# Performance work log

Hardware: AMD Instinct MI355X
Metric: run time of the kernel (lower is better)

## Reference

```python
import jax, jax.numpy as jnp
import numpy as np

B, T, D, H = 8, 1024, 768, 12
HD = D // H          # 64 head dim
WINDOW = 768         # sliding-window width hardcoded in the block
EPS = 1e-5

def _layer_norm(x, w, b):
    mu = jnp.mean(x, axis=-1, keepdims=True)
    var = jnp.mean(jnp.square(x - mu), axis=-1, keepdims=True)
    return (x - mu) * jax.lax.rsqrt(var + EPS) * w + b

def setup_inputs() -> dict:
    key = jax.random.key(0)
    ks = jax.random.split(key, 16)
    s = 0.02
    return {
        "x": jax.random.normal(ks[0], (B, T, D), jnp.float32),
        "attn_mask": jnp.ones((B, T), jnp.int32),
        "ln1_w": jnp.ones((D,), jnp.float32),
        "ln1_b": jnp.zeros((D,), jnp.float32),
        "w_attn": jax.random.normal(ks[1], (D, 3 * D), jnp.float32) * s,
        "b_attn": jnp.zeros((3 * D,), jnp.float32),
        "w_proj": jax.random.normal(ks[2], (D, D), jnp.float32) * s,
        "b_proj": jnp.zeros((D,), jnp.float32),
        "ln2_w": jnp.ones((D,), jnp.float32),
        "ln2_b": jnp.zeros((D,), jnp.float32),
        "w_fc": jax.random.normal(ks[3], (D, 4 * D), jnp.float32) * s,
        "b_fc": jnp.zeros((4 * D,), jnp.float32),
        "w_fc_proj": jax.random.normal(ks[4], (4 * D, D), jnp.float32) * s,
        "b_fc_proj": jnp.zeros((D,), jnp.float32),
    }

def reference(x, attn_mask, ln1_w, ln1_b, w_attn, b_attn, w_proj, b_proj,
              ln2_w, ln2_b, w_fc, b_fc, w_fc_proj, b_fc_proj):
    dtype = x.dtype
    # --- attention sub-block ---
    x1 = _layer_norm(x, ln1_w, ln1_b)
    qkv = x1 @ w_attn + b_attn                       # [B,T,3D]
    q, k, v = jnp.split(qkv, 3, axis=-1)
    q = q.reshape(B, T, H, HD).transpose(0, 2, 1, 3)  # [B,H,T,HD]
    k = k.reshape(B, T, H, HD).transpose(0, 2, 1, 3)
    v = v.reshape(B, T, H, HD).transpose(0, 2, 1, 3)
    # causal + sliding-window + padding mask (additive bias, as in source)
    i = jnp.arange(T)[:, None]
    j = jnp.arange(T)[None, :]
    keep = (j <= i) & (j >= i - WINDOW + 1)           # [T,T]
    keep = keep[None, None] & (attn_mask.astype(bool))[:, None, None, :]  # [B,1,T,T]
    mask_bias = jnp.where(keep, jnp.zeros((), dtype), jnp.full((), jnp.finfo(dtype).min, dtype))
    scale = 1.0 / np.sqrt(HD)
    scores = jnp.einsum('bhqd,bhkd->bhqk', q, k) * scale + mask_bias
    probs = jax.nn.softmax(scores, axis=-1)
    attn = jnp.einsum('bhqk,bhkd->bhqd', probs, v)    # [B,H,T,HD]
    attn = attn.transpose(0, 2, 1, 3).reshape(B, T, D)
    a = attn @ w_proj + b_proj
    x = x + a
    # --- MLP sub-block ---
    x3 = _layer_norm(x, ln2_w, ln2_b)
    h = jax.nn.gelu(x3 @ w_fc + b_fc, approximate=False)
    m = h @ w_fc_proj + b_fc_proj
    return x + m
```

## Files before the change

kernel.cpp:

```cpp
#include <hip/hip_runtime.h>
#include <hip/hip_bf16.h>
#include <math.h>

#define NB 8
#define NT 1024
#define ND 768
#define NH 12
#define HD 64
#define WINDOW 768
#define LN_EPS 1e-5f
#define NEGF -3.4028234663852886e38f
#define SCL2 0.18033688011112042f

static const int BT = NB * NT;

typedef __bf16 bf16x8 __attribute__((ext_vector_type(8)));
typedef float  f32x4  __attribute__((ext_vector_type(4)));
typedef unsigned short ushort_t;

__device__ __forceinline__ unsigned short f2bf(float f) {
    __hip_bfloat16 h = __float2bfloat16(f);
    return __builtin_bit_cast(unsigned short, h);
}

__device__ __forceinline__ void load_lds16(const void* g, void* l) {
    __builtin_amdgcn_global_load_lds((const __attribute__((address_space(1))) unsigned int*)g,
                                     (__attribute__((address_space(3))) unsigned int*)l,
                                     16, 0, 0);
}

__global__ __launch_bounds__(256) void transpose_all(const float* __restrict__ w0, ushort_t* __restrict__ t0v,
                                                     const float* __restrict__ w1, ushort_t* __restrict__ t1v,
                                                     const float* __restrict__ w2, ushort_t* __restrict__ t2v,
                                                     const float* __restrict__ w3, ushort_t* __restrict__ t3v) {
    int bid = blockIdx.x;
    const float* w; ushort_t* wt; int K, N;
    if (bid < 1728)                    { w = w0; wt = t0v; K = 768;  N = 2304; }
    else if ((bid -= 1728) < 576)      { w = w1; wt = t1v; K = 768;  N = 768;  }
    else if ((bid -= 576) < 2304)      { w = w2; wt = t2v; K = 768;  N = 3072; }
    else       { bid -= 2304;            w = w3; wt = t3v; K = 3072; N = 768;  }
    const int nxt = N / 32;
    const int n0 = (bid % nxt) * 32, k0 = (bid / nxt) * 32;
    __shared__ float t[32][33];
    const int tx = threadIdx.x & 31, ty = threadIdx.x >> 5;
    for (int r = ty; r < 32; r += 8)
        t[r][tx] = w[(size_t)(k0 + r) * N + n0 + tx];
    __syncthreads();
    for (int r = ty; r < 32; r += 8)
        wt[(size_t)(n0 + r) * K + k0 + tx] = f2bf(t[tx][r]);
}

__global__ __launch_bounds__(256) void transpose_v(const ushort_t* __restrict__ qkvb,
                                                   ushort_t* __restrict__ vT) {
    const int t0 = blockIdx.x * 64;
    const int h = blockIdx.y, b = blockIdx.z;
    __shared__ ushort_t sm[64 * 72];
    const int tid = threadIdx.x;
    #pragma unroll
    for (int p = 0; p < 2; p++) {
        int idx = p * 256 + tid;
        int r = idx >> 3, c = idx & 7;
        *(bf16x8*)&sm[r * 72 + c * 8] =
            *(const bf16x8*)(qkvb + (size_t)(b * NT + t0 + r) * (3 * ND) + 2 * ND + h * HD + c * 8);
    }
    __syncthreads();
    #pragma unroll
    for (int p = 0; p < 2; p++) {
        int idx = p * 256 + tid;
        int d = idx >> 3, c2 = idx & 7;
        ushort_t tmp[8];
        #pragma unroll
        for (int j = 0; j < 8; j++) {
            int kp = c2 * 8 + j;
            int key = ((kp & 1) << 4) | ((kp >> 1) & 15) | (kp & 32);
            tmp[j] = sm[key * 72 + d];
        }
        *(bf16x8*)(vT + ((size_t)((b * NH + h) * HD + d)) * NT + t0 + c2 * 8) = *(bf16x8*)tmp;
    }
}

__global__ __launch_bounds__(256) void ln_kernel(const float* __restrict__ x,
                                                 const float* __restrict__ w,
                                                 const float* __restrict__ b,
                                                 ushort_t* __restrict__ out) {
    const int row  = blockIdx.x * 4 + (threadIdx.x >> 6);
    const int lane = threadIdx.x & 63;
    const float* xr = x + (size_t)row * ND;

    float4 v[3];
    #pragma unroll
    for (int s = 0; s < 3; s++) v[s] = *(const float4*)(xr + s * 256 + lane * 4);

    float sum = 0.f;
    #pragma unroll
    for (int s = 0; s < 3; s++) sum += v[s].x + v[s].y + v[s].z + v[s].w;
    #pragma unroll
    for (int off = 1; off < 64; off <<= 1) sum += __shfl_xor(sum, off, 64);
    const float mu = sum * (1.0f / ND);

    float var = 0.f;
    #pragma unroll
    for (int s = 0; s < 3; s++) {
        float a0 = v[s].x - mu, a1 = v[s].y - mu, a2 = v[s].z - mu, a3 = v[s].w - mu;
        var += a0 * a0 + a1 * a1 + a2 * a2 + a3 * a3;
    }
    #pragma unroll
    for (int off = 1; off < 64; off <<= 1) var += __shfl_xor(var, off, 64);
    const float rstd = rsqrtf(var * (1.0f / ND) + LN_EPS);

    #pragma unroll
    for (int s = 0; s < 3; s++) {
        const int col = s * 256 + lane * 4;
        float4 w4 = *(const float4*)(w + col);
        float4 b4 = *(const float4*)(b + col);
        ushort4 r;
        r.x = f2bf((v[s].x - mu) * rstd * w4.x + b4.x);
        r.y = f2bf((v[s].y - mu) * rstd * w4.y + b4.y);
        r.z = f2bf((v[s].z - mu) * rstd * w4.z + b4.z);
        r.w = f2bf((v[s].w - mu) * rstd * w4.w + b4.w);
        *(ushort4*)(out + (size_t)row * ND + col) = r;
    }
}

template <int EPI>
__global__ __launch_bounds__(256) void gemm_bt(const ushort_t* __restrict__ A,
                                               const ushort_t* __restrict__ Bt,
                                               const float* __restrict__ bias,
                                               const float* __restrict__ resid,
                                               void* __restrict__ Cout,
                                               int M, int N, int K) {
    __shared__ __align__(16) ushort_t smem[2][2][128 * 32];

    const int tid  = threadIdx.x;
    const int bm   = blockIdx.y * 128;
    const int bn   = blockIdx.x * 128;
    const int lane = tid & 63;
    const int wave = tid >> 6;
    const int wm   = (wave & 1) * 64;
    const int wn   = (wave >> 1) * 64;
    const int fcol = lane & 15;
    const int quad = lane >> 4;

    f32x4 acc[4][4] = {};

    const int srow = tid >> 2, scg = (tid & 3) * 8;

    auto issue = [&](int k0, int buf) {
        #pragma unroll
        for (int p = 0; p < 2; p++) {
            const int row = srow + p * 64;
            const int flat = (p * 256 + tid) * 8;
            load_lds16(A  + (size_t)(bm + row) * K + k0 + scg, &smem[buf][0][flat]);
            load_lds16(Bt + (size_t)(bn + row) * K + k0 + scg, &smem[buf][1][flat]);
        }
    };

    issue(0, 0);
    const int KT = K >> 5;
    for (int kt = 0; kt < KT; kt++) {
        const int cur = kt & 1;
        __syncthreads();
        if (kt + 1 < KT) issue((kt + 1) << 5, cur ^ 1);

        bf16x8 a[4], b[4];
        #pragma unroll
        for (int i = 0; i < 4; i++)
            a[i] = *(const bf16x8*)&smem[cur][0][(wm + i * 16 + fcol) * 32 + quad * 8];
        #pragma unroll
        for (int j = 0; j < 4; j++)
            b[j] = *(const bf16x8*)&smem[cur][1][(wn + j * 16 + fcol) * 32 + quad * 8];
        #pragma unroll
        for (int i = 0; i < 4; i++)
            #pragma unroll
            for (int j = 0; j < 4; j++)
                acc[i][j] = __builtin_amdgcn_mfma_f32_16x16x32_bf16(a[i], b[j], acc[i][j], 0, 0, 0);
    }

    if (EPI == 1) {
        #pragma unroll
        for (int j = 0; j < 4; j++) {
            const int gcol = bn + wn + j * 16 + fcol;
            const float bs = bias[gcol];
            #pragma unroll
            for (int i = 0; i < 4; i++) {
                #pragma unroll
                for (int r = 0; r < 4; r++) {
                    const int grow = bm + wm + i * 16 + quad * 4 + r;
                    float val = acc[i][j][r] + bs + resid[(size_t)grow * N + gcol];
                    ((float*)Cout)[(size_t)grow * N + gcol] = val;
                }
            }
        }
    } else {
        __syncthreads();
        ushort_t* Cs = &smem[0][0][0] + wave * (64 * 40);
        #pragma unroll
        for (int hh = 0; hh < 2; hh++) {
            #pragma unroll
            for (int jj = 0; jj < 2; jj++) {
                const int j = hh * 2 + jj;
                const float bs = bias[bn + wn + j * 16 + fcol];
                #pragma unroll
                for (int i = 0; i < 4; i++) {
                    #pragma unroll
                    for (int r = 0; r < 4; r++) {
                        float val = acc[i][j][r] + bs;
                        if (EPI == 2) {
                            float y = 0.7978845608028654f * (val + 0.044715f * val * val * val);
                            float t = 1.0f - 2.0f / (1.0f + __expf(2.0f * y));
                            val = 0.5f * val * (1.0f + t);
                        }
                        const int lr = i * 16 + quad * 4 + r;
                        Cs[lr * 40 + jj * 16 + fcol] = f2bf(val);
                    }
                }
            }
            #pragma unroll
            for (int p = 0; p < 4; p++) {
                const int cid = p * 64 + lane;
                const int lr = cid >> 2, ck = cid & 3;
                bf16x8 vv = *(const bf16x8*)&Cs[lr * 40 + ck * 8];
                *(bf16x8*)((ushort_t*)Cout + (size_t)(bm + wm + lr) * N + bn + wn + hh * 32 + ck * 8) = vv;
            }
        }
    }
}

__global__ __launch_bounds__(256) void flash_attn_mfma(const ushort_t* __restrict__ qkvb,
                                                       const ushort_t* __restrict__ vT,
                                                       const int* __restrict__ amask,
                                                       ushort_t* __restrict__ out) {
    const int qt = 15 - blockIdx.x;
    const int h  = blockIdx.y;
    const int b  = blockIdx.z;
    const int q0 = qt * 64;

    __shared__ __align__(16) ushort_t QPs[64 * 64];
    __shared__ __align__(16) ushort_t Ks[2][64 * 64];
    __shared__ __align__(16) ushort_t Vts[2][64 * 64];

    const int tid  = threadIdx.x;
    const int lane = tid & 63;
    const int wave = tid >> 6;
    const int fcol = lane & 15;
    const int quad = lane >> 4;
    const int wq0  = wave * 16;

    #pragma unroll
    for (int p = 0; p < 2; p++) {
        int flat = p * 256 + tid;
        int r = flat >> 3, c = (flat & 7) ^ (r & 7);
        load_lds16(qkvb + (size_t)(b * NT + q0 + r) * (3 * ND) + h * HD + c * 8, &QPs[flat * 8]);
    }
    __syncthreads();

    bf16x8 aQ[2];
    {
        const int qr = wq0 + fcol;
        #pragma unroll
        for (int ks = 0; ks < 2; ks++) {
            int c = ks * 4 + quad;
            aQ[ks] = *(const bf16x8*)&QPs[qr * 64 + ((c ^ (qr & 7)) * 8)];
        }
    }

    bf16x8 bones;
    #pragma unroll
    for (int i = 0; i < 8; i++) bones[i] = (__bf16)1.0f;

    auto issueKV = [&](int cch, int buf) {
        const int kbase = cch * 64;
        #pragma unroll
        for (int p = 0; p < 2; p++) {
            int flat = p * 256 + tid;
            int r = flat >> 3, c = (flat & 7) ^ (r & 7);
            load_lds16(qkvb + (size_t)(b * NT + kbase + r) * (3 * ND) + ND + h * HD + c * 8,
                       &Ks[buf][flat * 8]);
            load_lds16(vT + ((size_t)((b * NH + h) * HD + r)) * NT + kbase + c * 8,
                       &Vts[buf][flat * 8]);
        }
    };

    f32x4 oacc[4] = {};
    f32x4 lacc = {};

    const int c_lo = (qt > 12) ? (qt - 12) : 0;
    issueKV(c_lo, 0);
    for (int cch = c_lo; cch <= qt; cch++) {
        const int cur = (cch - c_lo) & 1;
        const int kbase = cch * 64;
        __syncthreads();
        if (cch + 1 <= qt) issueKV(cch + 1, cur ^ 1);

        int am[4];
        #pragma unroll
        for (int jn = 0; jn < 4; jn++) am[jn] = amask[b * NT + kbase + jn * 16 + fcol];
        const int amok_lane = (am[0] != 0) & (am[1] != 0) & (am[2] != 0) & (am[3] != 0);
        const bool fast = (cch < qt) && (cch >= qt - 11) && __all(amok_lane);

        f32x4 sc[4] = {};
        #pragma unroll
        for (int ks = 0; ks < 2; ks++) {
            #pragma unroll
            for (int jn = 0; jn < 4; jn++) {
                const int kr = jn * 16 + fcol;
                bf16x8 bk = *(const bf16x8*)&Ks[cur][kr * 64 + (((ks * 4 + quad) ^ (kr & 7)) * 8)];
                sc[jn] = __builtin_amdgcn_mfma_f32_16x16x32_bf16(aQ[ks], bk, sc[jn], 0, 0, 0);
            }
        }

        float pvv[4][4];
        if (fast) {
            #pragma unroll
            for (int jn = 0; jn < 4; jn++)
                #pragma unroll
                for (int r = 0; r < 4; r++)
                    pvv[jn][r] = __builtin_amdgcn_exp2f(sc[jn][r] * SCL2);
        } else {
            #pragma unroll
            for (int jn = 0; jn < 4; jn++) {
                const int jg = kbase + jn * 16 + fcol;
                const bool amok = (am[jn] != 0);
                #pragma unroll
                for (int r = 0; r < 4; r++) {
                    const int ig = q0 + wq0 + quad * 4 + r;
                    bool keep = (jg <= ig) && (jg >= ig - (WINDOW - 1)) && amok;
                    float s = keep ? sc[jn][r] * SCL2 : -1e38f;
                    pvv[jn][r] = __builtin_amdgcn_exp2f(s);
                }
            }
        }

        #pragma unroll
        for (int half = 0; half < 2; half++) {
            const int cbase = half * 4 + (fcol >> 2);
            const int off = (fcol & 3) * 2;
            #pragma unroll
            for (int r = 0; r < 4; r++) {
                const int row = wq0 + quad * 4 + r;
                unsigned int pk = (unsigned int)f2bf(pvv[half * 2][r]) |
                                  ((unsigned int)f2bf(pvv[half * 2 + 1][r]) << 16);
                *(unsigned int*)&QPs[row * 64 + ((cbase ^ (row & 7)) * 8) + off] = pk;
            }
        }

        #pragma unroll
        for (int ks = 0; ks < 2; ks++) {
            const int pr = wq0 + fcol;
            bf16x8 ap = *(const bf16x8*)&QPs[pr * 64 + (((ks * 4 + quad) ^ (pr & 7)) * 8)];
            lacc = __builtin_amdgcn_mfma_f32_16x16x32_bf16(ap, bones, lacc, 0, 0, 0);
            #pragma unroll
            for (int jd = 0; jd < 4; jd++) {
                const int vr = jd * 16 + fcol;
                bf16x8 bv = *(const bf16x8*)&Vts[cur][vr * 64 + (((ks * 4 + quad) ^ (vr & 7)) * 8)];
                oacc[jd] = __builtin_amdgcn_mfma_f32_16x16x32_bf16(ap, bv, oacc[jd], 0, 0, 0);
            }
        }
    }

    #pragma unroll
    for (int r = 0; r < 4; r++) {
        const float inv = 1.0f / lacc[r];
        const size_t row = (size_t)(b * NT + q0 + wq0 + quad * 4 + r);
        #pragma unroll
        for (int jd = 0; jd < 4; jd++)
            out[row * ND + h * HD + jd * 16 + fcol] = f2bf(oacc[jd][r] * inv);
    }
}

extern "C" void kernel_launch(void* const* d_in, const int* in_sizes, int n_in,
                              void* d_out, int out_size, void* d_ws, size_t ws_size,
                              hipStream_t stream) {
    const float* x        = (const float*)d_in[0];
    const int*   amask    = (const int*)  d_in[1];
    const float* ln1_w    = (const float*)d_in[2];
    const float* ln1_b    = (const float*)d_in[3];
    const float* w_attn   = (const float*)d_in[4];
    const float* b_attn   = (const float*)d_in[5];
    const float* w_proj   = (const float*)d_in[6];
    const float* b_proj   = (const float*)d_in[7];
    const float* ln2_w    = (const float*)d_in[8];
    const float* ln2_b    = (const float*)d_in[9];
    const float* w_fc     = (const float*)d_in[10];
    const float* b_fc     = (const float*)d_in[11];
    const float* w_fcp    = (const float*)d_in[12];
    const float* b_fcp    = (const float*)d_in[13];
    float* out = (float*)d_out;

    ushort_t* ws = (ushort_t*)d_ws;
    ushort_t* qkvb   = ws;
    ushort_t* x1b    = qkvb + (size_t)BT * 3 * ND;
    ushort_t* attn_b = x1b + (size_t)BT * ND;
    ushort_t* hbuf   = attn_b + (size_t)BT * ND;
    ushort_t* vTb    = hbuf + (size_t)BT * 4 * ND;
    ushort_t* wA_T   = vTb + (size_t)BT * ND;
    ushort_t* wP_T   = wA_T + (size_t)2304 * 768;
    ushort_t* wF_T   = wP_T + (size_t)768 * 768;
    ushort_t* wFP_T  = wF_T + (size_t)3072 * 768;

    transpose_all<<<6912, 256, 0, stream>>>(w_attn, wA_T, w_proj, wP_T, w_fc, wF_T, w_fcp, wFP_T);

    ln_kernel<<<BT / 4, 256, 0, stream>>>(x, ln1_w, ln1_b, x1b);
    gemm_bt<0><<<dim3(2304 / 128, BT / 128), 256, 0, stream>>>(x1b, wA_T, b_attn, nullptr, qkvb, BT, 3 * ND, ND);
    transpose_v<<<dim3(16, NH, NB), 256, 0, stream>>>(qkvb, vTb);
    flash_attn_mfma<<<dim3(16, NH, NB), 256, 0, stream>>>(qkvb, vTb, amask, attn_b);
    gemm_bt<1><<<dim3(768 / 128, BT / 128), 256, 0, stream>>>(attn_b, wP_T, b_proj, x, out, BT, ND, ND);
    ln_kernel<<<BT / 4, 256, 0, stream>>>(out, ln2_w, ln2_b, x1b);
    gemm_bt<2><<<dim3(3072 / 128, BT / 128), 256, 0, stream>>>(x1b, wF_T, b_fc, nullptr, hbuf, BT, 4 * ND, ND);
    gemm_bt<1><<<dim3(768 / 128, BT / 128), 256, 0, stream>>>(hbuf, wFP_T, b_fcp, out, out, BT, ND, 4 * ND);
}
```

Baseline: 393.4 us.

## Add 256x256-tile 8-wave pipelined GEMM for QKV and FC layers

Adds a new GEMM kernel with 256x256 output tiles, 512 threads, and 128KB of dynamic LDS. It uses swizzled async global-to-LDS loads double-buffered across K steps, interleaved with MFMA phases under setprio and barriers. It replaces the 128x128 gemm_bt for the QKV projection and the FC+GELU layers, to raise data reuse per tile and overlap loads with compute. The trade-off is fewer blocks (for example 9x32 for QKV), which may underfill the GPU, plus high register and LDS pressure.

```diff
diff --git a/kernel.cpp b/kernel.cpp
--- a/kernel.cpp
+++ b/kernel.cpp
@@ -226,6 +226,152 @@
     }
 }
 
+template <int EPI>
+__global__ __launch_bounds__(512, 2) void gemm256(const ushort_t* __restrict__ A,
+                                                  const ushort_t* __restrict__ Bt,
+                                                  const float* __restrict__ bias,
+                                                  ushort_t* __restrict__ Cout,
+                                                  int N, int K) {
+    extern __shared__ __align__(16) ushort_t lds[];
+
+    const int tid  = threadIdx.x;
+    const int lane = tid & 63;
+    const int wave = tid >> 6;
+    const int wr   = wave >> 2;
+    const int wn   = wave & 3;
+    const int fcol = lane & 15;
+    const int quad = lane >> 4;
+    const int bm   = blockIdx.y * 256;
+    const int bn   = blockIdx.x * 256;
+    const int KT   = K >> 6;
+    const int NIT  = KT >> 1;
+
+    f32x4 acc[8][4] = {};
+    bf16x8 ra[4][2];
+    bf16x8 rb0[2][2], rb1[2][2];
+
+    ushort_t* const Ab = lds;
+    ushort_t* const Bb = lds + 32768;
+
+    auto stA = [&](int kt, int h) {
+        ushort_t* dst = Ab + ((((kt & 1) << 1) | h) << 13);
+        const int kk = (kt < KT ? kt : 0) << 6;
+        #pragma unroll
+        for (int p = 0; p < 2; p++) {
+            const int f = (p << 9) + tid;
+            const int r = f >> 3, c = (f & 7) ^ (r & 7);
+            const int gr = bm + ((r >> 6) << 7) + (h << 6) + (r & 63);
+            load_lds16(A + (size_t)gr * K + kk + c * 8, dst + f * 8);
+        }
+    };
+    auto stB = [&](int kt, int h) {
+        ushort_t* dst = Bb + ((((kt & 1) << 1) | h) << 13);
+        const int kk = (kt < KT ? kt : 0) << 6;
+        #pragma unroll
+        for (int p = 0; p < 2; p++) {
+            const int f = (p << 9) + tid;
+            const int r = f >> 3, c = (f & 7) ^ (r & 7);
+            const int gr = bn + ((r >> 5) << 6) + (h << 5) + (r & 31);
+            load_lds16(Bt + (size_t)gr * K + kk + c * 8, dst + f * 8);
+        }
+    };
+
+#define SOFF(r, c) ((((r) << 3) + (((c) ^ ((r) & 7)))) << 3)
+#define LOAD_A(PAR, MH) { ushort_t* s_ = Ab + ((((PAR) << 1) | (MH)) << 13);        \
+    _Pragma("unroll") for (int i2 = 0; i2 < 4; i2++)                                 \
+    _Pragma("unroll") for (int ks = 0; ks < 2; ks++)                                 \
+        ra[i2][ks] = *(const bf16x8*)&s_[SOFF(wr * 64 + i2 * 16 + fcol, ks * 4 + quad)]; }
+#define LOAD_B(PAR, NH, RB) { ushort_t* s_ = Bb + ((((PAR) << 1) | (NH)) << 13);     \
+    _Pragma("unroll") for (int j2 = 0; j2 < 2; j2++)                                 \
+    _Pragma("unroll") for (int ks = 0; ks < 2; ks++)                                 \
+        RB[j2][ks] = *(const bf16x8*)&s_[SOFF(wn * 32 + j2 * 16 + fcol, ks * 4 + quad)]; }
+#define MMA(MH, NH, RB) { __builtin_amdgcn_s_setprio(1);                             \
+    _Pragma("unroll") for (int i2 = 0; i2 < 4; i2++)                                 \
+    _Pragma("unroll") for (int j2 = 0; j2 < 2; j2++)                                 \
+    _Pragma("unroll") for (int ks = 0; ks < 2; ks++)                                 \
+        acc[(MH) * 4 + i2][(NH) * 2 + j2] = __builtin_amdgcn_mfma_f32_16x16x32_bf16( \
+            ra[i2][ks], RB[j2][ks], acc[(MH) * 4 + i2][(NH) * 2 + j2], 0, 0, 0);     \
+    __builtin_amdgcn_s_setprio(0); }
+#define BAR() __builtin_amdgcn_s_barrier()
+
+    stA(0, 0); stB(0, 0); stB(0, 1); stA(0, 1);
+    stA(1, 0); stB(1, 0); stB(1, 1);
+    asm volatile("s_waitcnt vmcnt(6)" ::: "memory");
+    BAR();
+
+    for (int it = 0; it < NIT; ++it) {
+        const int E = it << 1, O = E + 1;
+        LOAD_A(0, 0); LOAD_B(0, 0, rb0);
+        stA(O, 1);
+        BAR(); MMA(0, 0, rb0); BAR();
+
+        LOAD_B(0, 1, rb1);
+        stA(E + 2, 0);
+        BAR(); MMA(0, 1, rb1); BAR();
+
+        LOAD_A(0, 1);
+        stB(E + 2, 0);
+        BAR(); MMA(1, 1, rb1); BAR();
+
+        stB(E + 2, 1);
+        asm volatile("s_waitcnt vmcnt(6)" ::: "memory");
+        BAR(); MMA(1, 0, rb0); BAR();
+
+        LOAD_A(1, 0); LOAD_B(1, 0, rb0);
+        stA(E + 2, 1);
+        BAR(); MMA(0, 0, rb0); BAR();
+
+        LOAD_B(1, 1, rb1);
+        stA(O + 2, 0);
+        BAR(); MMA(0, 1, rb1); BAR();
+
+        LOAD_A(1, 1);
+        stB(O + 2, 0);
+        BAR(); MMA(1, 1, rb1); BAR();
+
+        stB(O + 2, 1);
+        asm volatile("s_waitcnt vmcnt(6)" ::: "memory");
+        BAR(); MMA(1, 0, rb0); BAR();
+    }
+
+    asm volatile("s_waitcnt vmcnt(0)" ::: "memory");
+    BAR();
+
+    ushort_t* Cs = lds + wave * (64 * 72);
+    #pragma unroll
+    for (int h = 0; h < 2; h++) {
+        #pragma unroll
+        for (int j = 0; j < 4; j++) {
+            const float bs = bias[bn + wn * 64 + j * 16 + fcol];
+            #pragma unroll
+            for (int i2 = 0; i2 < 4; i2++) {
+                #pragma unroll
+                for (int r = 0; r < 4; r++) {
+                    float val = acc[h * 4 + i2][j][r] + bs;
+                    if (EPI == 2) {
+                        float y = 0.7978845608028654f * (val + 0.044715f * val * val * val);
+                        float t = 1.0f - 2.0f / (1.0f + __expf(2.0f * y));
+                        val = 0.5f * val * (1.0f + t);
+                    }
+                    Cs[(i2 * 16 + quad * 4 + r) * 72 + j * 16 + fcol] = f2bf(val);
+                }
+            }
+        }
+        #pragma unroll
+        for (int p = 0; p < 8; p++) {
+            const int cid = (p << 6) + lane;
+            const int lr = cid >> 3, ck = cid & 7;
+            bf16x8 vv = *(const bf16x8*)&Cs[lr * 72 + ck * 8];
+            *(bf16x8*)(Cout + (size_t)(bm + wr * 128 + h * 64 + lr) * N + bn + wn * 64 + ck * 8) = vv;
+        }
+    }
+#undef SOFF
+#undef LOAD_A
+#undef LOAD_B
+#undef MMA
+#undef BAR
+}
+
 __global__ __launch_bounds__(256) void flash_attn_mfma(const ushort_t* __restrict__ qkvb,
                                                        const ushort_t* __restrict__ vT,
                                                        const int* __restrict__ amask,
@@ -398,14 +544,21 @@
     ushort_t* wF_T   = wP_T + (size_t)768 * 768;
     ushort_t* wFP_T  = wF_T + (size_t)3072 * 768;
 
+    static bool attr_set = false;
+    if (!attr_set) {
+        hipFuncSetAttribute((const void*)gemm256<0>, hipFuncAttributeMaxDynamicSharedMemorySize, 131072);
+        hipFuncSetAttribute((const void*)gemm256<2>, hipFuncAttributeMaxDynamicSharedMemorySize, 131072);
+        attr_set = true;
+    }
+
     transpose_all<<<6912, 256, 0, stream>>>(w_attn, wA_T, w_proj, wP_T, w_fc, wF_T, w_fcp, wFP_T);
 
     ln_kernel<<<BT / 4, 256, 0, stream>>>(x, ln1_w, ln1_b, x1b);
-    gemm_bt<0><<<dim3(2304 / 128, BT / 128), 256, 0, stream>>>(x1b, wA_T, b_attn, nullptr, qkvb, BT, 3 * ND, ND);
+    gemm256<0><<<dim3(2304 / 256, BT / 256), 512, 131072, stream>>>(x1b, wA_T, b_attn, qkvb, 3 * ND, ND);
     transpose_v<<<dim3(16, NH, NB), 256, 0, stream>>>(qkvb, vTb);
     flash_attn_mfma<<<dim3(16, NH, NB), 256, 0, stream>>>(qkvb, vTb, amask, attn_b);
     gemm_bt<1><<<dim3(768 / 128, BT / 128), 256, 0, stream>>>(attn_b, wP_T, b_proj, x, out, BT, ND, ND);
     ln_kernel<<<BT / 4, 256, 0, stream>>>(out, ln2_w, ln2_b, x1b);
-    gemm_bt<2><<<dim3(3072 / 128, BT / 128), 256, 0, stream>>>(x1b, wF_T, b_fc, nullptr, hbuf, BT, 4 * ND, ND);
+    gemm256<2><<<dim3(3072 / 256, BT / 256), 512, 131072, stream>>>(x1b, wF_T, b_fc, hbuf, 4 * ND, ND);
     gemm_bt<1><<<dim3(768 / 128, BT / 128), 256, 0, stream>>>(hbuf, wFP_T, b_fcp, out, out, BT, ND, 4 * ND);
 }
```

Measured after the change: 386.2 us. Within noise of the previous version (-1.8%).

## Add 128x256 swizzled-LDS GEMM kernel for QKV and FC layers

Applied to the files above, without the earlier changes.

Adds a new 512-thread GEMM kernel with 128x256 tiles, XOR-swizzled LDS layout, hand-scheduled ds_read with immediate offsets, explicit waitcnt/barrier double buffering and setprio around MFMA blocks. It replaces the QKV and FC GEMMs; the existing gemm_bt also gains an XCD-aware block index swizzle. The aim is higher operand reuse per LDS tile, fewer bank conflicts and better L2 locality across chiplets, at the cost of more fragile manual synchronisation and higher register and LDS pressure.

```diff
diff --git a/kernel.cpp b/kernel.cpp
--- a/kernel.cpp
+++ b/kernel.cpp
@@ -27,6 +27,13 @@
     __builtin_amdgcn_global_load_lds((const __attribute__((address_space(1))) unsigned int*)g,
                                      (__attribute__((address_space(3))) unsigned int*)l,
                                      16, 0, 0);
+}
+
+template <int IMM>
+__device__ __forceinline__ bf16x8 ds_read16o(unsigned base) {
+    bf16x8 r;
+    asm volatile("ds_read_b128 %0, %1 offset:%2" : "=v"(r) : "v"(base), "n"(IMM));
+    return r;
 }
 
 __global__ __launch_bounds__(256) void transpose_all(const float* __restrict__ w0, ushort_t* __restrict__ t0v,
@@ -132,8 +139,12 @@
     __shared__ __align__(16) ushort_t smem[2][2][128 * 32];
 
     const int tid  = threadIdx.x;
-    const int bm   = blockIdx.y * 128;
-    const int bn   = blockIdx.x * 128;
+    const int nwg   = gridDim.x * gridDim.y;
+    const int flatb = blockIdx.y * gridDim.x + blockIdx.x;
+    const int q8    = nwg >> 3;
+    const int swz   = (flatb & 7) * q8 + (flatb >> 3);
+    const int bm   = (swz / gridDim.x) * 128;
+    const int bn   = (swz % gridDim.x) * 128;
     const int lane = tid & 63;
     const int wave = tid >> 6;
     const int wm   = (wave & 1) * 64;
@@ -224,6 +235,140 @@
             }
         }
     }
+}
+
+template <int EPI, int NN, int KK>
+__global__ __launch_bounds__(512, 4) void gemm128n(const ushort_t* __restrict__ A,
+                                                   const ushort_t* __restrict__ Bt,
+                                                   const float* __restrict__ bias,
+                                                   ushort_t* __restrict__ Cout) {
+    __shared__ __align__(16) ushort_t lds[24576];
+
+    const int tid  = threadIdx.x;
+    const int lane = tid & 63;
+    const int wave = tid >> 6;
+    const int wr   = wave >> 2;
+    const int wn   = wave & 3;
+    const int fcol = lane & 15;
+    const int quad = lane >> 4;
+
+    const int nwg   = gridDim.x * gridDim.y;
+    const int flatb = blockIdx.y * gridDim.x + blockIdx.x;
+    const int q8    = nwg >> 3;
+    const int swz   = (flatb & 7) * q8 + (flatb >> 3);
+    const int bm    = (swz / gridDim.x) * 128;
+    const int bn    = (swz % gridDim.x) * 256;
+
+    constexpr int KTILES = KK >> 5;
+
+    f32x4 acc[4][4] = {};
+    bf16x8 ra[4], rbv[4];
+
+    const unsigned ldsb = (unsigned)(size_t)(const __attribute__((address_space(3))) ushort_t*)lds;
+    const unsigned sw   = (unsigned)((quad ^ (fcol & 3)) * 16);
+    const unsigned baseA = ldsb + (unsigned)((wr * 64 + fcol) * 64) + sw;
+    const unsigned baseB = ldsb + 16384u + (unsigned)((wn * 64 + fcol) * 64) + sw;
+
+    auto stage = [&](int kt) {
+        const int kk = (kt < KTILES ? kt : 0) << 5;
+        ushort_t* dstA = lds + (kt & 1) * 4096;
+        {
+            const int f = tid;
+            const int r = f >> 2, c = (f & 3) ^ (r & 3);
+            load_lds16(A + (size_t)(bm + r) * KK + kk + c * 8, dstA + f * 8);
+        }
+        ushort_t* dstB = lds + 8192 + (kt & 1) * 8192;
+        #pragma unroll
+        for (int p = 0; p < 2; p++) {
+            const int f = (p << 9) + tid;
+            const int r = f >> 2, c = (f & 3) ^ (r & 3);
+            load_lds16(Bt + (size_t)(bn + r) * KK + kk + c * 8, dstB + f * 8);
+        }
+    };
+
+#define RD_T(CUR) {                                                        \
+    ra[0]  = ds_read16o<(CUR) * 8192 + 0   >(baseA);                       \
+    ra[1]  = ds_read16o<(CUR) * 8192 + 1024>(baseA);                       \
+    ra[2]  = ds_read16o<(CUR) * 8192 + 2048>(baseA);                       \
+    ra[3]  = ds_read16o<(CUR) * 8192 + 3072>(baseA);                       \
+    rbv[0] = ds_read16o<(CUR) * 16384 + 0   >(baseB);                      \
+    rbv[1] = ds_read16o<(CUR) * 16384 + 1024>(baseB);                      \
+    rbv[2] = ds_read16o<(CUR) * 16384 + 2048>(baseB);                      \
+    rbv[3] = ds_read16o<(CUR) * 16384 + 3072>(baseB); }
+#define LGKM0() { asm volatile("s_waitcnt lgkmcnt(0)" ::: "memory");       \
+    __builtin_amdgcn_sched_barrier(0); }
+#define MMA16() {                                                          \
+    __builtin_amdgcn_s_setprio(1);                                         \
+    _Pragma("unroll") for (int i = 0; i < 4; i++)                          \
+    _Pragma("unroll") for (int j = 0; j < 4; j++)                          \
+        acc[i][j] = __builtin_amdgcn_mfma_f32_16x16x32_bf16(               \
+            ra[i], rbv[j], acc[i][j], 0, 0, 0);                            \
+    __builtin_amdgcn_s_setprio(0);                                         \
+    __builtin_amdgcn_sched_barrier(0); }
+#define VMW3() asm volatile("s_waitcnt vmcnt(3)" ::: "memory")
+#define BARR() asm volatile("s_barrier" ::: "memory")
+
+    stage(0); stage(1);
+    VMW3();
+    BARR();
+
+    #pragma unroll 1
+    for (int it = 0; it < KTILES / 2; ++it) {
+        const int t = it << 1;
+        RD_T(0);
+        LGKM0();
+        MMA16();
+        BARR();
+        stage(t + 2);
+        VMW3();
+        BARR();
+        RD_T(1);
+        LGKM0();
+        MMA16();
+        BARR();
+        stage(t + 3);
+        VMW3();
+        BARR();
+    }
+
+    asm volatile("s_waitcnt vmcnt(0) lgkmcnt(0)" ::: "memory");
+    BARR();
+
+    ushort_t* Cs = lds + wave * (32 * 72);
+    #pragma unroll
+    for (int h = 0; h < 2; h++) {
+        #pragma unroll
+        for (int j = 0; j < 4; j++) {
+            const float bs = bias[bn + wn * 64 + j * 16 + fcol];
+            #pragma unroll
+            for (int i2 = 0; i2 < 2; i2++) {
+                #pragma unroll
+                for (int r = 0; r < 4; r++) {
+                    float val = acc[h * 2 + i2][j][r] + bs;
+                    if (EPI == 2) {
+                        float y = 0.7978845608028654f * (val + 0.044715f * val * val * val);
+                        float t = 1.0f - 2.0f / (1.0f + __expf(2.0f * y));
+                        val = 0.5f * val * (1.0f + t);
+                    }
+                    Cs[(i2 * 16 + quad * 4 + r) * 72 + j * 16 + fcol] = f2bf(val);
+                }
+            }
+        }
+        __builtin_amdgcn_sched_barrier(0);
+        #pragma unroll
+        for (int p = 0; p < 4; p++) {
+            const int cid = (p << 6) + lane;
+            const int lr = cid >> 3, ck = cid & 7;
+            bf16x8 vv = *(const bf16x8*)&Cs[lr * 72 + ck * 8];
+            *(bf16x8*)(Cout + (size_t)(bm + wr * 64 + h * 32 + lr) * NN + bn + wn * 64 + ck * 8) = vv;
+        }
+        __builtin_amdgcn_sched_barrier(0);
+    }
+#undef RD_T
+#undef LGKM0
+#undef MMA16
+#undef VMW3
+#undef BARR
 }
 
 __global__ __launch_bounds__(256) void flash_attn_mfma(const ushort_t* __restrict__ qkvb,
@@ -401,11 +546,11 @@
     transpose_all<<<6912, 256, 0, stream>>>(w_attn, wA_T, w_proj, wP_T, w_fc, wF_T, w_fcp, wFP_T);
 
     ln_kernel<<<BT / 4, 256, 0, stream>>>(x, ln1_w, ln1_b, x1b);
-    gemm_bt<0><<<dim3(2304 / 128, BT / 128), 256, 0, stream>>>(x1b, wA_T, b_attn, nullptr, qkvb, BT, 3 * ND, ND);
+    gemm128n<0, 2304, 768><<<dim3(2304 / 256, BT / 128), 512, 0, stream>>>(x1b, wA_T, b_attn, qkvb);
     transpose_v<<<dim3(16, NH, NB), 256, 0, stream>>>(qkvb, vTb);
     flash_attn_mfma<<<dim3(16, NH, NB), 256, 0, stream>>>(qkvb, vTb, amask, attn_b);
     gemm_bt<1><<<dim3(768 / 128, BT / 128), 256, 0, stream>>>(attn_b, wP_T, b_proj, x, out, BT, ND, ND);
     ln_kernel<<<BT / 4, 256, 0, stream>>>(out, ln2_w, ln2_b, x1b);
-    gemm_bt<2><<<dim3(3072 / 128, BT / 128), 256, 0, stream>>>(x1b, wF_T, b_fc, nullptr, hbuf, BT, 4 * ND, ND);
+    gemm128n<2, 3072, 768><<<dim3(3072 / 256, BT / 128), 512, 0, stream>>>(x1b, wF_T, b_fc, hbuf);
     gemm_bt<1><<<dim3(768 / 128, BT / 128), 256, 0, stream>>>(hbuf, wFP_T, b_fcp, out, out, BT, ND, 4 * ND);
 }
```

Measured after the change: 351.8 us. 10.6% less time.
